# Optimization experiments

Measured on AMD Instinct MI355X. Metric: run time of the kernel, lower is better.

Reference implementation:

```python
import jax, jax.numpy as jnp
import numpy as np

B, T, HID = 1, 2048, 1024
H, D, S, KMAX = 16, 64, 64, 8


def local_attention(q, k, v, W):
    # lucidrains LocalAttention: causal, look_backward=1, autopad, scale=D**-0.5
    b, h, t, d = q.shape
    pad = (-t) % W
    qp = jnp.pad(q, ((0, 0), (0, 0), (0, pad), (0, 0)))
    kp = jnp.pad(k, ((0, 0), (0, 0), (0, pad), (0, 0)))
    vp = jnp.pad(v, ((0, 0), (0, 0), (0, pad), (0, 0)))
    tp = t + pad
    nw = tp // W
    qw = qp.reshape(b, h, nw, W, d)
    kw = kp.reshape(b, h, nw, W, d)
    vw = vp.reshape(b, h, nw, W, d)

    def look_back(x):  # prepend previous window (zeros for window 0)
        prev = jnp.pad(x, ((0, 0), (0, 0), (1, 0), (0, 0), (0, 0)))[:, :, :nw]
        return jnp.concatenate([prev, x], axis=3)  # (b,h,nw,2W,d)

    kk, vv = look_back(kw), look_back(vw)
    pos = jnp.arange(tp).reshape(nw, W)
    kpos = jnp.concatenate(
        [jnp.pad(pos, ((1, 0), (0, 0)), constant_values=-1)[:nw], pos], axis=1)  # (nw,2W)
    scores = jnp.einsum('bhnwd,bhnkd->bhnwk', qw, kk) * (d ** -0.5)
    valid = (pos[:, :, None] >= kpos[:, None, :]) & (kpos[:, None, :] >= 0)
    scores = jnp.where(valid[None, None], scores, -jnp.finfo(scores.dtype).max)
    probs = jax.nn.softmax(scores, axis=-1)
    out = jnp.einsum('bhnwk,bhnkd->bhnwd', probs, vv).reshape(b, h, tp, d)
    return out[:, :, :t]


def setup_inputs() -> dict:
    key = jax.random.key(0)
    ks = jax.random.split(key, 9)
    sd = 0.02
    return {
        'hidden_states': jax.random.normal(ks[0], (B, T, HID), jnp.float32),
        'Wq': jax.random.normal(ks[1], (HID, H * D), jnp.float32) * sd,
        'Wk': jax.random.normal(ks[2], (HID, H * D), jnp.float32) * sd,
        'Wv': jax.random.normal(ks[3], (HID, H * D), jnp.float32) * sd,
        'Wo': jax.random.normal(ks[4], (H * D, HID), jnp.float32) * sd,
        'Wc': jax.random.normal(ks[5], (S * D, D), jnp.float32) * sd,
        'bc': jax.random.normal(ks[6], (D,), jnp.float32) * sd,
        'k_scale': jnp.ones((1, H, 1), jnp.float32),
        'k_bias': jnp.zeros((1, H, 1), jnp.float32),
        'Wg': jax.random.normal(ks[7], (HID, 3 * H), jnp.float32) * sd,
        'bg': jax.random.normal(ks[8], (3 * H,), jnp.float32) * sd,
    }


def reference(hidden_states, Wq, Wk, Wv, Wo, Wc, bc, k_scale, k_bias, Wg, bg):
    b, t, _ = hidden_states.shape
    scale = D ** -0.5
    q = (hidden_states @ Wq).reshape(b, t, H, D).transpose(0, 2, 1, 3)
    k = (hidden_states @ Wk).reshape(b, t, H, D).transpose(0, 2, 1, 3)
    v = (hidden_states @ Wv).reshape(b, t, H, D).transpose(0, 2, 1, 3)

    sw_out = local_attention(q, k, v, S)

    pad = (-t) % S
    qp = jnp.pad(q, ((0, 0), (0, 0), (0, pad), (0, 0)))
    kp = jnp.pad(k, ((0, 0), (0, 0), (0, pad), (0, 0)))
    vp = jnp.pad(v, ((0, 0), (0, 0), (0, pad), (0, 0)))
    tp = t + pad
    nb = tp // S

    # compressed branch: shared compress MLP for k and v (same weights in torch)
    k_blk = kp.reshape(b, H, nb, S * D)
    v_blk = vp.reshape(b, H, nb, S * D)
    kc = jax.nn.gelu(k_blk @ Wc + bc, approximate=False)  # (b,H,nb,D)
    vc = jax.nn.gelu(v_blk @ Wc + bc, approximate=False)

    importance = jnp.einsum('bhid,bhjd->bhij', qp, kc) * scale  # (b,H,tp,nb)
    comp_probs = jax.nn.softmax(importance, axis=-1)
    comp_out = jnp.einsum('bhij,bhjd->bhid', comp_probs, vc)[:, :, :t]

    # block scores, entropy-driven dynamic top-k
    block_scores = importance.reshape(b, H, nb, S, nb).mean(axis=3)  # (b,H,nb,nb)
    block_probs = jax.nn.softmax(block_scores, axis=-1)
    entropy = -jnp.sum(block_probs * jnp.log(block_probs + 1e-9), axis=-1)
    max_entropy = jnp.log(jnp.float32(nb))
    norm_entropy = entropy / (max_entropy + 1e-9)  # (b,H,nb)
    k_logit = k_scale * norm_entropy + k_bias
    k_ratio = jax.nn.sigmoid(k_logit)
    dynamic_k = jnp.clip(KMAX * k_ratio, 1, KMAX).astype(jnp.int32)
    avg_k = dynamic_k.astype(jnp.float32).mean()

    _, topk_idx = jax.lax.top_k(block_scores, KMAX)  # (b,H,nb,KMAX)
    k_mask = jnp.arange(KMAX)[None, None, None, :] < dynamic_k[..., None]
    sel = (topk_idx[..., None] == jnp.arange(nb)) & k_mask[..., None]  # (b,H,nb,K,nb)
    mask = sel.any(axis=-2) | jnp.eye(nb, dtype=bool)  # (b,H,nb,nb)
    sparse_mask = jnp.repeat(jnp.repeat(mask, S, axis=2), S, axis=3)  # (b,H,tp,tp)

    attn = jnp.einsum('bhid,bhjd->bhij', qp, kp) * scale
    attn = jnp.where(sparse_mask, attn, -jnp.finfo(attn.dtype).max)
    fine_probs = jax.nn.softmax(attn, axis=-1)
    fine_out = jnp.einsum('bhij,bhjd->bhid', fine_probs, vp)[:, :, :t]

    gate = jax.nn.sigmoid(hidden_states @ Wg + bg)  # (b,t,3H)
    gate = gate.reshape(b, t, H, 3).transpose(0, 2, 1, 3)  # (b,H,t,3)
    combined = jnp.stack([sw_out, comp_out, fine_out], axis=-1)  # (b,H,t,D,3)
    out = jnp.einsum('bhnds,bhns->bhnd', combined, gate)
    merged = out.transpose(0, 2, 1, 3).reshape(b, t, H * D)
    output = merged @ Wo
    return output, avg_k, k_ratio, norm_entropy
```

## Files before the change

kernel.cpp:

```cpp
#include <hip/hip_runtime.h>
#include <math.h>

#define TT 2048
#define NH 16
#define HD 64
#define NB 32
#define HIDDEN 1024

typedef short s8v __attribute__((ext_vector_type(8)));
typedef float f4v __attribute__((ext_vector_type(4)));

__device__ __forceinline__ unsigned short f2bf(float x){
  unsigned u = __float_as_uint(x);
  unsigned r = (u + 0x7fffu + ((u>>16)&1u)) >> 16;
  return (unsigned short)r;
}
__device__ __forceinline__ float bf2f(unsigned short b){
  return __uint_as_float(((unsigned)b)<<16);
}
__device__ __forceinline__ void bsplit(float x, unsigned short& h, unsigned short& l){
  h = f2bf(x);
  l = f2bf(x - bf2f(h));
}

__device__ __forceinline__ float rmax32(float v){
#pragma unroll
  for(int o=16;o>0;o>>=1) v = fmaxf(v, __shfl_xor(v,o,32));
  return v;
}
__device__ __forceinline__ float rsum32(float v){
#pragma unroll
  for(int o=16;o>0;o>>=1) v += __shfl_xor(v,o,32);
  return v;
}

__global__ __launch_bounds__(256) void prep_all(
    const float* __restrict__ hs,
    const float* __restrict__ Wq, const float* __restrict__ Wk,
    const float* __restrict__ Wv, const float* __restrict__ Wo,
    const float* __restrict__ Wc,
    const float* __restrict__ Wg, const float* __restrict__ bg,
    unsigned short* __restrict__ hh, unsigned short* __restrict__ hl,
    unsigned short* __restrict__ wth, unsigned short* __restrict__ wtl,
    unsigned short* __restrict__ woth,
    unsigned short* __restrict__ wcth, unsigned short* __restrict__ wctl,
    float* __restrict__ gatep)
{
  __shared__ float SL[64*68];
  int bx = blockIdx.x;
  int t = threadIdx.x;
  if(bx < 2048){
    int i = (bx*256 + t)*4;
    float4 x = *(const float4*)(hs + i);
    ushort4 hv, lv;
    bsplit(x.x, hv.x, lv.x); bsplit(x.y, hv.y, lv.y);
    bsplit(x.z, hv.z, lv.z); bsplit(x.w, hv.w, lv.w);
    *(ushort4*)(hh + i) = hv;
    *(ushort4*)(hl + i) = lv;
    return;
  }
  if(bx < 3072){
    float (*L)[68] = (float(*)[68])SL;
    int idx = bx - 2048;
    int z = idx>>8, ky = (idx>>4)&15, nx = idx&15;
    const float* W = (z==0)?Wq:((z==1)?Wk:((z==2)?Wv:Wo));
    int k0 = ky*64, n0 = nx*64;
    int rr = t>>2, cg = t&3;
    const float* src = W + (size_t)(k0+rr)*1024 + n0 + cg*16;
    float4 a = *(const float4*)(src);
    float4 b = *(const float4*)(src+4);
    float4 c = *(const float4*)(src+8);
    float4 d = *(const float4*)(src+12);
    *(float4*)&L[rr][cg*16+0]  = a;
    *(float4*)&L[rr][cg*16+4]  = b;
    *(float4*)&L[rr][cg*16+8]  = c;
    *(float4*)&L[rr][cg*16+12] = d;
    __syncthreads();
    int nr = t>>2, kg = t&3;
    unsigned short hb[16], lb[16];
#pragma unroll
    for(int j=0;j<16;j++){
      float v = L[kg*16+j][nr];
      bsplit(v, hb[j], lb[j]);
    }
    if(z<3){
      size_t orow = ((size_t)z*1024 + n0 + nr)*1024 + k0 + kg*16;
      *(ushort4*)(wth+orow+0)  = make_ushort4(hb[0],hb[1],hb[2],hb[3]);
      *(ushort4*)(wth+orow+4)  = make_ushort4(hb[4],hb[5],hb[6],hb[7]);
      *(ushort4*)(wth+orow+8)  = make_ushort4(hb[8],hb[9],hb[10],hb[11]);
      *(ushort4*)(wth+orow+12) = make_ushort4(hb[12],hb[13],hb[14],hb[15]);
      *(ushort4*)(wtl+orow+0)  = make_ushort4(lb[0],lb[1],lb[2],lb[3]);
      *(ushort4*)(wtl+orow+4)  = make_ushort4(lb[4],lb[5],lb[6],lb[7]);
      *(ushort4*)(wtl+orow+8)  = make_ushort4(lb[8],lb[9],lb[10],lb[11]);
      *(ushort4*)(wtl+orow+12) = make_ushort4(lb[12],lb[13],lb[14],lb[15]);
    }else{
      size_t orow = ((size_t)n0 + nr)*1024 + k0 + kg*16;
      *(ushort4*)(woth+orow+0)  = make_ushort4(hb[0],hb[1],hb[2],hb[3]);
      *(ushort4*)(woth+orow+4)  = make_ushort4(hb[4],hb[5],hb[6],hb[7]);
      *(ushort4*)(woth+orow+8)  = make_ushort4(hb[8],hb[9],hb[10],hb[11]);
      *(ushort4*)(woth+orow+12) = make_ushort4(hb[12],hb[13],hb[14],hb[15]);
    }
    return;
  }
  if(bx < 3136){
    float (*L)[68] = (float(*)[68])SL;
    int k0 = (bx - 3072)*64;
    int rr = t>>2, cg = t&3;
    const float* src = Wc + (size_t)(k0+rr)*64 + cg*16;
    float4 a = *(const float4*)(src);
    float4 b = *(const float4*)(src+4);
    float4 c = *(const float4*)(src+8);
    float4 d = *(const float4*)(src+12);
    *(float4*)&L[rr][cg*16+0]  = a;
    *(float4*)&L[rr][cg*16+4]  = b;
    *(float4*)&L[rr][cg*16+8]  = c;
    *(float4*)&L[rr][cg*16+12] = d;
    __syncthreads();
    int nr = t>>2, kg = t&3;
    unsigned short hb[16], lb[16];
#pragma unroll
    for(int j=0;j<16;j++){
      float v = L[kg*16+j][nr];
      bsplit(v, hb[j], lb[j]);
    }
    size_t orow = (size_t)nr*4096 + k0 + kg*16;
    *(ushort4*)(wcth+orow+0)  = make_ushort4(hb[0],hb[1],hb[2],hb[3]);
    *(ushort4*)(wcth+orow+4)  = make_ushort4(hb[4],hb[5],hb[6],hb[7]);
    *(ushort4*)(wcth+orow+8)  = make_ushort4(hb[8],hb[9],hb[10],hb[11]);
    *(ushort4*)(wcth+orow+12) = make_ushort4(hb[12],hb[13],hb[14],hb[15]);
    *(ushort4*)(wctl+orow+0)  = make_ushort4(lb[0],lb[1],lb[2],lb[3]);
    *(ushort4*)(wctl+orow+4)  = make_ushort4(lb[4],lb[5],lb[6],lb[7]);
    *(ushort4*)(wctl+orow+8)  = make_ushort4(lb[8],lb[9],lb[10],lb[11]);
    *(ushort4*)(wctl+orow+12) = make_ushort4(lb[12],lb[13],lb[14],lb[15]);
    return;
  }
  {
    float* row = SL;
    float (*red)[64] = (float(*)[64])(SL + 1024);
    int tr = bx - 3136;
    *(float4*)(row + t*4) = *(const float4*)(hs + (size_t)tr*HIDDEN + t*4);
    __syncthreads();
    int n = t & 63, part = t>>6;
    float s = 0.f;
    if(n < 48){
      const float* w = Wg + n;
      for(int kx = part*256; kx < part*256+256; kx++)
        s += row[kx]*w[(size_t)kx*48];
    }
    red[part][n] = s;
    __syncthreads();
    if(part==0 && n<48){
      float x = red[0][n]+red[1][n]+red[2][n]+red[3][n] + bg[n];
      gatep[(size_t)tr*48 + n] = 1.f/(1.f+expf(-x));
    }
  }
}

#define LROW 40
__global__ __launch_bounds__(256) void mfma_qkv_k(
    const unsigned short* __restrict__ ahg, const unsigned short* __restrict__ alg,
    const unsigned short* __restrict__ bhg, const unsigned short* __restrict__ blg,
    unsigned short* __restrict__ qbh, unsigned short* __restrict__ qbl,
    unsigned short* __restrict__ kbh, unsigned short* __restrict__ kbl,
    unsigned short* __restrict__ vbh)
{
  __shared__ unsigned short SH[15360];
  unsigned short* SA  = SH;
  unsigned short* SAl = SH + 5120;
  unsigned short* SB  = SH + 10240;
  unsigned short* SBl = SH + 12800;
  int tid = threadIdx.x;
  int bn = blockIdx.x*64, bm = blockIdx.y*128;
  bool tp = (blockIdx.x < 32);
  int aRow = tid>>1, aOff = (tid&1)*16;
  int bRow = tid>>2, bOff = (tid&3)*8;
  const unsigned short* gA  = ahg + (size_t)(bm+aRow)*HIDDEN + aOff;
  const unsigned short* gAl = alg + (size_t)(bm+aRow)*HIDDEN + aOff;
  const unsigned short* gB  = bhg + (size_t)(bn+bRow)*HIDDEN + bOff;
  const unsigned short* gBl = blg + (size_t)(bn+bRow)*HIDDEN + bOff;
  int wlA = aRow*LROW + aOff;
  int wlB = bRow*LROW + bOff;
  int wv = tid>>6, ln = tid&63;
  int wm = (wv&1)*64, wn = (wv>>1)*32;
  int fr = ln&15, fq = ln>>4;
  f4v acc[4][2] = {};
  for(int k0=0;k0<HIDDEN;k0+=32){
    s8v a0 = *(const s8v*)(gA + k0);
    s8v a1 = *(const s8v*)(gA + k0 + 8);
    s8v b0 = *(const s8v*)(gB + k0);
    s8v a0l, a1l, b0l;
    if(tp){
      a0l = *(const s8v*)(gAl + k0);
      a1l = *(const s8v*)(gAl + k0 + 8);
      b0l = *(const s8v*)(gBl + k0);
    }
    __syncthreads();
    *(s8v*)&SA[wlA] = a0; *(s8v*)&SA[wlA+8] = a1;
    *(s8v*)&SB[wlB] = b0;
    if(tp){
      *(s8v*)&SAl[wlA] = a0l; *(s8v*)&SAl[wlA+8] = a1l;
      *(s8v*)&SBl[wlB] = b0l;
    }
    __syncthreads();
    s8v af[4], bf[2], tf;
#pragma unroll
    for(int i=0;i<4;i++) af[i] = *(const s8v*)&SA[(wm+i*16+fr)*LROW + fq*8];
#pragma unroll
    for(int j=0;j<2;j++) bf[j] = *(const s8v*)&SB[(wn+j*16+fr)*LROW + fq*8];
#pragma unroll
    for(int i=0;i<4;i++)
#pragma unroll
      for(int j=0;j<2;j++)
        acc[i][j] = __builtin_amdgcn_mfma_f32_16x16x32_bf16(af[i], bf[j], acc[i][j], 0,0,0);
    if(tp){
#pragma unroll
      for(int i=0;i<4;i++){
        tf = *(const s8v*)&SAl[(wm+i*16+fr)*LROW + fq*8];
#pragma unroll
        for(int j=0;j<2;j++)
          acc[i][j] = __builtin_amdgcn_mfma_f32_16x16x32_bf16(tf, bf[j], acc[i][j], 0,0,0);
      }
#pragma unroll
      for(int j=0;j<2;j++){
        tf = *(const s8v*)&SBl[(wn+j*16+fr)*LROW + fq*8];
#pragma unroll
        for(int i=0;i<4;i++)
          acc[i][j] = __builtin_amdgcn_mfma_f32_16x16x32_bf16(af[i], tf, acc[i][j], 0,0,0);
      }
    }
  }
  int z = bn >> 10;
  int head = (bn & 1023) >> 6;
  unsigned short* Cs = SH;
  unsigned short* dsth = (z==0)?qbh:((z==1)?kbh:vbh);
  size_t obase = ((size_t)head*TT + bm)*HD;
  __syncthreads();
#pragma unroll
  for(int i=0;i<4;i++)
#pragma unroll
    for(int j=0;j<2;j++)
#pragma unroll
      for(int r=0;r<4;r++)
        Cs[(wm+i*16+fq*4+r)*64 + wn+j*16+fr] = f2bf(acc[i][j][r]);
  __syncthreads();
#pragma unroll
  for(int u=0;u<4;u++){
    int c = u*256 + tid;
    *(s8v*)(dsth + obase + c*8) = *(const s8v*)&Cs[c*8];
  }
  if(z<2){
    unsigned short* dstl = (z==0)?qbl:kbl;
    __syncthreads();
#pragma unroll
    for(int i=0;i<4;i++)
#pragma unroll
      for(int j=0;j<2;j++)
#pragma unroll
        for(int r=0;r<4;r++){
          float v = acc[i][j][r];
          Cs[(wm+i*16+fq*4+r)*64 + wn+j*16+fr] = f2bf(v - bf2f(f2bf(v)));
        }
    __syncthreads();
#pragma unroll
    for(int u=0;u<4;u++){
      int c = u*256 + tid;
      *(s8v*)(dstl + obase + c*8) = *(const s8v*)&Cs[c*8];
    }
  }
}

__global__ __launch_bounds__(256) void conv_vt(
    const unsigned short* __restrict__ vbh, unsigned short* __restrict__ vth)
{
  int tt = blockIdx.x, h = blockIdx.y;
  __shared__ unsigned short L[64][72];
  int t = threadIdx.x;
  int row = t>>2, dg = (t&3)*16;
  const unsigned short* src = vbh + ((size_t)h*TT + tt*64 + row)*HD + dg;
  *(s8v*)&L[row][dg]   = *(const s8v*)(src);
  *(s8v*)&L[row][dg+8] = *(const s8v*)(src+8);
  __syncthreads();
  int d = t>>2, kg = (t&3)*16;
  s8v r0, r1;
#pragma unroll
  for(int u=0;u<8;u++)  r0[u] = (short)L[kg+u][d];
#pragma unroll
  for(int u=0;u<8;u++)  r1[u] = (short)L[kg+8+u][d];
  unsigned short* dst = vth + ((size_t)h*HD + d)*TT + tt*64 + kg;
  *(s8v*)(dst)   = r0;
  *(s8v*)(dst+8) = r1;
}

#define CROW 40
__global__ __launch_bounds__(256) void mfma_compress_k(
    const unsigned short* __restrict__ kbh, const unsigned short* __restrict__ kbl,
    const unsigned short* __restrict__ vbh,
    const unsigned short* __restrict__ wcth, const unsigned short* __restrict__ wctl,
    float* __restrict__ ccpart)
{
  __shared__ unsigned short As[64*CROW], Al[64*CROW], Bs[64*CROW], Bl[64*CROW];
  int chunk = blockIdx.x;
  int mt = blockIdx.y;
  bool isK = (mt < 8);
  const unsigned short* Ag  = isK ? (kbh + (size_t)mt*262144) : (vbh + (size_t)(mt-8)*262144);
  const unsigned short* Agl = kbl + (size_t)(isK ? mt : 0)*262144;
  int tid = threadIdx.x;
  int sr = tid>>2, skg = (tid&3)*8;
  int k0b = chunk*512;
  const unsigned short* gA  = Ag  + (size_t)sr*4096 + k0b + skg;
  const unsigned short* gAl = Agl + (size_t)sr*4096 + k0b + skg;
  const unsigned short* gB  = wcth + (size_t)sr*4096 + k0b + skg;
  const unsigned short* gBl = wctl + (size_t)sr*4096 + k0b + skg;
  int wv = tid>>6, ln = tid&63;
  int fr = ln&15, fq = ln>>4;
  int wlds = sr*CROW + skg;
  f4v acc[4] = {};
  for(int ks=0; ks<512; ks+=32){
    s8v a0 = *(const s8v*)(gA + ks);
    s8v b0 = *(const s8v*)(gB + ks);
    s8v b1 = *(const s8v*)(gBl + ks);
    s8v a1 = {};
    if(isK) a1 = *(const s8v*)(gAl + ks);
    __syncthreads();
    *(s8v*)&As[wlds] = a0;
    *(s8v*)&Bs[wlds] = b0;
    *(s8v*)&Bl[wlds] = b1;
    if(isK) *(s8v*)&Al[wlds] = a1;
    __syncthreads();
    s8v bfh = *(const s8v*)&Bs[(wv*16+fr)*CROW + fq*8];
    s8v bfl = *(const s8v*)&Bl[(wv*16+fr)*CROW + fq*8];
#pragma unroll
    for(int m=0;m<4;m++){
      s8v af = *(const s8v*)&As[(m*16+fr)*CROW + fq*8];
      acc[m] = __builtin_amdgcn_mfma_f32_16x16x32_bf16(af, bfh, acc[m], 0,0,0);
      acc[m] = __builtin_amdgcn_mfma_f32_16x16x32_bf16(af, bfl, acc[m], 0,0,0);
      if(isK){
        s8v afl = *(const s8v*)&Al[(m*16+fr)*CROW + fq*8];
        acc[m] = __builtin_amdgcn_mfma_f32_16x16x32_bf16(afl, bfh, acc[m], 0,0,0);
      }
    }
  }
  float* dst = ccpart + ((size_t)chunk*1024 + mt*64)*64;
#pragma unroll
  for(int m=0;m<4;m++)
#pragma unroll
    for(int r=0;r<4;r++)
      dst[(size_t)(m*16+fq*4+r)*64 + wv*16 + fr] = acc[m][r];
}

__global__ __launch_bounds__(256) void compress_fin(
    const float* __restrict__ ccpart, const float* __restrict__ bcp,
    unsigned short* __restrict__ kch, unsigned short* __restrict__ kcl,
    unsigned short* __restrict__ vcth)
{
  int idx = blockIdx.x*256 + threadIdx.x;
  int row = idx>>6, col = idx&63;
  float s = 0.f;
#pragma unroll
  for(int c=0;c<8;c++) s += ccpart[(size_t)c*65536 + idx];
  s += bcp[col];
  float g = 0.5f*s*(1.f+erff(s*0.70710678118654752f));
  if(row < 512){
    unsigned short hi = f2bf(g);
    kch[idx] = hi;
    kcl[idx] = f2bf(g - bf2f(hi));
  }else{
    int r = row - 512;
    int h = r>>5, j = r&31;
    vcth[((size_t)h*64 + col)*32 + j] = f2bf(g);
  }
}

__global__ __launch_bounds__(256) void comp_attn_mfma(
    const unsigned short* __restrict__ qbh, const unsigned short* __restrict__ qbl,
    const unsigned short* __restrict__ kch, const unsigned short* __restrict__ kcl,
    const unsigned short* __restrict__ vcth,
    float* __restrict__ imp, float* __restrict__ comp)
{
  __shared__ unsigned short Pl[4*16*40];
  int tid = threadIdx.x;
  int wave = __builtin_amdgcn_readfirstlane(tid>>6);
  int ln = tid&63;
  int fr = ln&15, fq = ln>>4;
  int i = blockIdx.x, h = blockIdx.y;

  const unsigned short* qrh = qbh + ((size_t)h*TT + i*64 + wave*16 + fr)*HD + fq*8;
  const unsigned short* qrl = qbl + ((size_t)h*TT + i*64 + wave*16 + fr)*HD + fq*8;
  s8v bh0 = *(const s8v*)(qrh);
  s8v bh1 = *(const s8v*)(qrh + 32);
  s8v bl0 = *(const s8v*)(qrl);
  s8v bl1 = *(const s8v*)(qrl + 32);

  f4v sv[2] = {};
#pragma unroll
  for(int mt=0;mt<2;mt++){
    const unsigned short* ar = kch + ((size_t)h*32 + mt*16 + fr)*HD + fq*8;
    const unsigned short* al = kcl + ((size_t)h*32 + mt*16 + fr)*HD + fq*8;
    s8v ah0 = *(const s8v*)(ar);
    s8v ah1 = *(const s8v*)(ar + 32);
    s8v al0 = *(const s8v*)(al);
    s8v al1 = *(const s8v*)(al + 32);
    sv[mt] = __builtin_amdgcn_mfma_f32_16x16x32_bf16(ah0, bh0, sv[mt], 0,0,0);
    sv[mt] = __builtin_amdgcn_mfma_f32_16x16x32_bf16(ah1, bh1, sv[mt], 0,0,0);
    sv[mt] = __builtin_amdgcn_mfma_f32_16x16x32_bf16(al0, bh0, sv[mt], 0,0,0);
    sv[mt] = __builtin_amdgcn_mfma_f32_16x16x32_bf16(al1, bh1, sv[mt], 0,0,0);
    sv[mt] = __builtin_amdgcn_mfma_f32_16x16x32_bf16(ah0, bl0, sv[mt], 0,0,0);
    sv[mt] = __builtin_amdgcn_mfma_f32_16x16x32_bf16(ah1, bl1, sv[mt], 0,0,0);
  }
  int t = i*64 + wave*16 + fr;
  float* impr = imp + ((size_t)h*TT + t)*NB;
  float mx = -3.4e38f;
#pragma unroll
  for(int mt=0;mt<2;mt++)
#pragma unroll
    for(int r=0;r<4;r++){
      float s = sv[mt][r]*0.125f;
      sv[mt][r] = s;
      impr[mt*16 + fq*4 + r] = s;
      mx = fmaxf(mx, s);
    }
  mx = fmaxf(mx, __shfl_xor(mx,16,64));
  mx = fmaxf(mx, __shfl_xor(mx,32,64));
  unsigned short* Pw = Pl + wave*16*40;
  float es = 0.f;
#pragma unroll
  for(int mt=0;mt<2;mt++)
#pragma unroll
    for(int r=0;r<4;r++){
      float p = __expf(sv[mt][r] - mx);
      es += p;
      Pw[fr*40 + mt*16 + fq*4 + r] = f2bf(p);
    }
  es += __shfl_xor(es,16,64);
  es += __shfl_xor(es,32,64);

  s8v ap = *(const s8v*)&Pw[fr*40 + fq*8];
  f4v acc[4] = {};
#pragma unroll
  for(int nt=0;nt<4;nt++){
    s8v bv = *(const s8v*)(vcth + ((size_t)h*64 + nt*16 + fr)*32 + fq*8);
    acc[nt] = __builtin_amdgcn_mfma_f32_16x16x32_bf16(ap, bv, acc[nt], 0,0,0);
  }
  float lv[4];
#pragma unroll
  for(int r=0;r<4;r++) lv[r] = __shfl(es, fq*4+r, 64);
#pragma unroll
  for(int nt=0;nt<4;nt++)
#pragma unroll
    for(int r=0;r<4;r++){
      int tq = i*64 + wave*16 + fq*4 + r;
      comp[((size_t)h*TT + tq)*HD + nt*16 + fr] = acc[nt][r]/lv[r];
    }
}

__global__ __launch_bounds__(256) void block_stats(
    const float* __restrict__ imp, const float* __restrict__ ksc, const float* __restrict__ kbi,
    unsigned* __restrict__ maskb, float* __restrict__ dkf,
    float* __restrict__ out_kratio, float* __restrict__ out_nent)
{
  int hb = blockIdx.x; int h = hb>>5, i = hb&31;
  int tid = threadIdx.x; int j = tid&31, p = tid>>5;
  const float* base = imp + ((size_t)h*TT + i*64)*NB;
  float s = 0.f;
  for(int t2=p*8; t2<p*8+8; t2++) s += base[(size_t)t2*NB + j];
  __shared__ float red[8][32];
  red[p][j] = s;
  __syncthreads();
  if(tid < 32){
    float bs = 0.f;
#pragma unroll
    for(int pp=0; pp<8; pp++) bs += red[pp][j];
    bs *= (1.f/64.f);
    float m = rmax32(bs);
    float e = expf(bs - m);
    float se = rsum32(e);
    float prob = e/se;
    float ent = rsum32(-prob * logf(prob + 1e-9f));
    float nent = ent / (3.4657359027997265f + 1e-9f);
    float kl = ksc[h]*nent + kbi[h];
    float kr = 1.f/(1.f + expf(-kl));
    float dkfl = fminf(fmaxf(8.f*kr, 1.f), 8.f);
    int dk = (int)dkfl;
    unsigned sel = 0u;
    for(int r=0;r<dk;r++){
      bool unpicked = ((sel>>j)&1u)==0u;
      float cand = unpicked ? bs : -3.4e38f;
      float mx = rmax32(cand);
      unsigned long long b = __ballot(cand == mx);
      int idxsel = __ffsll(b & 0xffffffffull) - 1;
      sel |= (1u<<idxsel);
    }
    sel |= (1u<<i);
    if(j==0){
      maskb[hb] = sel;
      dkf[hb] = (float)dk;
      out_kratio[hb] = kr;
      out_nent[hb] = nent;
    }
  }
}

__global__ __launch_bounds__(256) void avgk_kernel(const float* __restrict__ dkf, float* __restrict__ outp){
  __shared__ float red[256];
  int tid=threadIdx.x;
  red[tid] = dkf[tid] + dkf[tid+256];
  __syncthreads();
  for(int s=128;s>0;s>>=1){ if(tid<s) red[tid]+=red[tid+s]; __syncthreads(); }
  if(tid==0) outp[0] = red[0] * (1.f/512.f);
}

__global__ __launch_bounds__(256) void attn_fused(
    const unsigned short* __restrict__ qbh, const unsigned short* __restrict__ kbh,
    const unsigned short* __restrict__ vth, const unsigned* __restrict__ maskb,
    const float* __restrict__ comp, const float* __restrict__ gatep,
    unsigned short* __restrict__ mergedh)
{
  __shared__ unsigned short Kb[64*72];
  __shared__ unsigned short Vt[64*72];
  __shared__ unsigned short Pf[4*16*72];
  __shared__ unsigned short Ps[4*16*72];
  int tid = threadIdx.x;
  int wave = __builtin_amdgcn_readfirstlane(tid>>6);
  int ln = tid & 63;
  int fr = ln & 15, fq = ln >> 4;
  int hb = blockIdx.x; int h = hb>>5, i = hb&31;
  unsigned mb_s = (1u<<i) | (i ? (1u<<(i-1)) : 0u);
  unsigned mb_f = maskb[hb];
  unsigned mb = mb_s | mb_f;

  const unsigned short* qrow = qbh + ((size_t)h*TT + i*64 + wave*16 + fr)*HD + fq*8;
  s8v bq0 = *(const s8v*)(qrow);
  s8v bq1 = *(const s8v*)(qrow + 32);

  f4v acc_f[4] = {}, acc_s[4] = {};
  float mf = -3.4e38f, lf = 0.f, ms = -3.4e38f, ls = 0.f;

  int srow = tid>>2, sg = (tid&3)*16;
  unsigned short* Pfw = Pf + wave*16*72;
  unsigned short* Psw = Ps + wave*16*72;
  int qpos = wave*16 + fr;

  for(int j=0;j<NB;j++){
    if(!((mb>>j)&1u)) continue;
    __syncthreads();
    {
      const unsigned short* ks_ = kbh + ((size_t)h*TT + j*64 + srow)*HD + sg;
      *(s8v*)&Kb[srow*72 + sg]     = *(const s8v*)(ks_);
      *(s8v*)&Kb[srow*72 + sg + 8] = *(const s8v*)(ks_ + 8);
      const unsigned short* vs_ = vth + ((size_t)h*HD + srow)*TT + j*64 + sg;
      *(s8v*)&Vt[srow*72 + sg]     = *(const s8v*)(vs_);
      *(s8v*)&Vt[srow*72 + sg + 8] = *(const s8v*)(vs_ + 8);
    }
    __syncthreads();

    f4v sv[4] = {};
#pragma unroll
    for(int mt=0;mt<4;mt++){
      s8v ak0 = *(const s8v*)&Kb[(mt*16+fr)*72 + fq*8];
      s8v ak1 = *(const s8v*)&Kb[(mt*16+fr)*72 + fq*8 + 32];
      sv[mt] = __builtin_amdgcn_mfma_f32_16x16x32_bf16(ak0, bq0, sv[mt], 0,0,0);
      sv[mt] = __builtin_amdgcn_mfma_f32_16x16x32_bf16(ak1, bq1, sv[mt], 0,0,0);
    }
#pragma unroll
    for(int mt=0;mt<4;mt++)
#pragma unroll
      for(int r=0;r<4;r++) sv[mt][r] *= 0.125f;

    bool in_f = ((mb_f>>j)&1u) != 0u;
    bool in_s = (j==i) || (j+1==i);

    if(in_f){
      float mx = -3.4e38f;
#pragma unroll
      for(int mt=0;mt<4;mt++)
#pragma unroll
        for(int r=0;r<4;r++) mx = fmaxf(mx, sv[mt][r]);
      mx = fmaxf(mx, __shfl_xor(mx,16,64));
      mx = fmaxf(mx, __shfl_xor(mx,32,64));
      float mnew = fmaxf(mf, mx);
      float es = 0.f;
#pragma unroll
      for(int mt=0;mt<4;mt++)
#pragma unroll
        for(int r=0;r<4;r++){
          float p = __expf(sv[mt][r] - mnew);
          es += p;
          Pfw[fr*72 + mt*16 + fq*4 + r] = f2bf(p);
        }
      es += __shfl_xor(es,16,64);
      es += __shfl_xor(es,32,64);
      float alpha = __expf(mf - mnew);
      lf = lf*alpha + es;
      mf = mnew;
      float av[4];
#pragma unroll
      for(int r=0;r<4;r++) av[r] = __shfl(alpha, fq*4+r, 64);
#pragma unroll
      for(int nt=0;nt<4;nt++)
#pragma unroll
        for(int r=0;r<4;r++) acc_f[nt][r] *= av[r];
    }
    if(in_s){
      if(j==i){
#pragma unroll
        for(int mt=0;mt<4;mt++)
#pragma unroll
          for(int r=0;r<4;r++)
            if((mt*16 + fq*4 + r) > qpos) sv[mt][r] = -3.4e38f;
      }
      float mx = -3.4e38f;
#pragma unroll
      for(int mt=0;mt<4;mt++)
#pragma unroll
        for(int r=0;r<4;r++) mx = fmaxf(mx, sv[mt][r]);
      mx = fmaxf(mx, __shfl_xor(mx,16,64));
      mx = fmaxf(mx, __shfl_xor(mx,32,64));
      float mnew = fmaxf(ms, mx);
      float es = 0.f;
#pragma unroll
      for(int mt=0;mt<4;mt++)
#pragma unroll
        for(int r=0;r<4;r++){
          float p = __expf(sv[mt][r] - mnew);
          es += p;
          Psw[fr*72 + mt*16 + fq*4 + r] = f2bf(p);
        }
      es += __shfl_xor(es,16,64);
      es += __shfl_xor(es,32,64);
      float alpha = __expf(ms - mnew);
      ls = ls*alpha + es;
      ms = mnew;
      float av[4];
#pragma unroll
      for(int r=0;r<4;r++) av[r] = __shfl(alpha, fq*4+r, 64);
#pragma unroll
      for(int nt=0;nt<4;nt++)
#pragma unroll
        for(int r=0;r<4;r++) acc_s[nt][r] *= av[r];
    }

    if(in_f){
      s8v ap0 = *(const s8v*)&Pfw[fr*72 + fq*8];
      s8v ap1 = *(const s8v*)&Pfw[fr*72 + fq*8 + 32];
#pragma unroll
      for(int nt=0;nt<4;nt++){
        s8v bv0 = *(const s8v*)&Vt[(nt*16+fr)*72 + fq*8];
        s8v bv1 = *(const s8v*)&Vt[(nt*16+fr)*72 + fq*8 + 32];
        acc_f[nt] = __builtin_amdgcn_mfma_f32_16x16x32_bf16(ap0, bv0, acc_f[nt], 0,0,0);
        acc_f[nt] = __builtin_amdgcn_mfma_f32_16x16x32_bf16(ap1, bv1, acc_f[nt], 0,0,0);
      }
    }
    if(in_s){
      s8v ap0 = *(const s8v*)&Psw[fr*72 + fq*8];
      s8v ap1 = *(const s8v*)&Psw[fr*72 + fq*8 + 32];
#pragma unroll
      for(int nt=0;nt<4;nt++){
        s8v bv0 = *(const s8v*)&Vt[(nt*16+fr)*72 + fq*8];
        s8v bv1 = *(const s8v*)&Vt[(nt*16+fr)*72 + fq*8 + 32];
        acc_s[nt] = __builtin_amdgcn_mfma_f32_16x16x32_bf16(ap0, bv0, acc_s[nt], 0,0,0);
        acc_s[nt] = __builtin_amdgcn_mfma_f32_16x16x32_bf16(ap1, bv1, acc_s[nt], 0,0,0);
      }
    }
  }

  float lvf[4], lvs[4], g0[4], g1[4], g2[4];
#pragma unroll
  for(int r=0;r<4;r++){
    lvf[r] = __shfl(lf, fq*4+r, 64);
    lvs[r] = __shfl(ls, fq*4+r, 64);
    int t = i*64 + wave*16 + fq*4 + r;
    const float* g = gatep + (size_t)t*48 + h*3;
    g0[r] = g[0]; g1[r] = g[1]; g2[r] = g[2];
  }
#pragma unroll
  for(int nt=0;nt<4;nt++){
#pragma unroll
    for(int r=0;r<4;r++){
      int t = i*64 + wave*16 + fq*4 + r;
      int d = nt*16 + fr;
      float of = acc_f[nt][r] / lvf[r];
      float os = acc_s[nt][r] / lvs[r];
      float cp = comp[((size_t)h*TT + t)*HD + d];
      mergedh[(size_t)t*1024 + h*64 + d] = f2bf(g0[r]*os + g1[r]*cp + g2[r]*of);
    }
  }
}

__global__ __launch_bounds__(256) void mfma_proj_k(
    const unsigned short* __restrict__ ahg, const unsigned short* __restrict__ bhg,
    float* __restrict__ C)
{
  __shared__ unsigned short SA[128*LROW], SB[64*LROW];
  int tid = threadIdx.x;
  int bn = blockIdx.x*64, bm = blockIdx.y*128;
  int aRow = tid>>1, aOff = (tid&1)*16;
  int bRow = tid>>2, bOff = (tid&3)*8;
  const unsigned short* gA = ahg + (size_t)(bm+aRow)*HIDDEN + aOff;
  const unsigned short* gB = bhg + (size_t)(bn+bRow)*HIDDEN + bOff;
  int wlA = aRow*LROW + aOff;
  int wlB = bRow*LROW + bOff;
  int wv = tid>>6, ln = tid&63;
  int wm = (wv&1)*64, wn = (wv>>1)*32;
  int fr = ln&15, fq = ln>>4;
  f4v acc[4][2] = {};
  for(int k0=0;k0<HIDDEN;k0+=32){
    s8v a0 = *(const s8v*)(gA + k0);
    s8v a1 = *(const s8v*)(gA + k0 + 8);
    s8v b0 = *(const s8v*)(gB + k0);
    __syncthreads();
    *(s8v*)&SA[wlA] = a0; *(s8v*)&SA[wlA+8] = a1;
    *(s8v*)&SB[wlB] = b0;
    __syncthreads();
    s8v af[4], bf[2];
#pragma unroll
    for(int i=0;i<4;i++) af[i] = *(const s8v*)&SA[(wm+i*16+fr)*LROW + fq*8];
#pragma unroll
    for(int j=0;j<2;j++) bf[j] = *(const s8v*)&SB[(wn+j*16+fr)*LROW + fq*8];
#pragma unroll
    for(int i=0;i<4;i++)
#pragma unroll
      for(int j=0;j<2;j++)
        acc[i][j] = __builtin_amdgcn_mfma_f32_16x16x32_bf16(af[i], bf[j], acc[i][j], 0,0,0);
  }
#pragma unroll
  for(int i=0;i<4;i++){
    int mb = bm + wm + i*16 + fq*4;
#pragma unroll
    for(int j=0;j<2;j++){
      int n = bn + wn + j*16 + fr;
      float* dst = C + (size_t)mb*HIDDEN + n;
#pragma unroll
      for(int r=0;r<4;r++) dst[(size_t)r*HIDDEN] = acc[i][j][r];
    }
  }
}

extern "C" void kernel_launch(void* const* d_in, const int* in_sizes, int n_in,
                              void* d_out, int out_size, void* d_ws, size_t ws_size,
                              hipStream_t stream) {
  (void)in_sizes; (void)n_in; (void)out_size; (void)ws_size;
  const float* hs  = (const float*)d_in[0];
  const float* Wq  = (const float*)d_in[1];
  const float* Wk  = (const float*)d_in[2];
  const float* Wv  = (const float*)d_in[3];
  const float* Wo  = (const float*)d_in[4];
  const float* Wc  = (const float*)d_in[5];
  const float* bcp = (const float*)d_in[6];
  const float* ksc = (const float*)d_in[7];
  const float* kbi = (const float*)d_in[8];
  const float* Wg  = (const float*)d_in[9];
  const float* bg  = (const float*)d_in[10];
  float* out = (float*)d_out;

  float* ws = (float*)d_ws;
  float* gatep  = ws;
  unsigned short* kch  = (unsigned short*)(gatep + 98304);
  unsigned short* kcl  = kch + 32768;
  unsigned short* vcth = kcl + 32768;
  float* imp    = gatep + 98304 + 65536;
  float* comp   = imp + 1048576;
  float* wthf   = comp + 2097152;
  float* wtlf   = wthf + 1572864;
  unsigned short* mergedh = (unsigned short*)(wtlf + 1572864);
  float* dkf    = wtlf + 1572864 + 1048576;
  unsigned* maskb = (unsigned*)(dkf + 512);
  unsigned short* woth = (unsigned short*)(dkf + 1024);
  unsigned short* qbh  = (unsigned short*)(dkf + 1024 + 524288);
  unsigned short* qbl  = qbh + 2097152;
  unsigned short* kbh  = qbl + 2097152;
  unsigned short* kbl  = kbh + 2097152;
  unsigned short* vbh  = kbl + 2097152;
  unsigned short* vth  = vbh + 2097152;
  unsigned short* wcth = vth + 2097152;
  unsigned short* wctl = wcth + 262144;
  float* ccpart = (float*)(wctl + 262144);

  unsigned short* hsh = (unsigned short*)comp;
  unsigned short* hsl = (unsigned short*)(comp + 1048576);
  unsigned short* wth = (unsigned short*)wthf;
  unsigned short* wtl = (unsigned short*)wtlf;

  float* out_avgk   = out + 2097152;
  float* out_kratio = out + 2097153;
  float* out_nent   = out + 2097665;

  prep_all<<<dim3(5184), 256, 0, stream>>>(hs, Wq, Wk, Wv, Wo, Wc, Wg, bg,
                                           hsh, hsl, wth, wtl, woth, wcth, wctl, gatep);
  mfma_qkv_k<<<dim3(48,16), 256, 0, stream>>>(hsh, hsl, wth, wtl,
                                              qbh, qbl, kbh, kbl, vbh);
  conv_vt<<<dim3(32,16), 256, 0, stream>>>(vbh, vth);
  mfma_compress_k<<<dim3(8,16), 256, 0, stream>>>(kbh, kbl, vbh, wcth, wctl, ccpart);
  compress_fin<<<dim3(256), 256, 0, stream>>>(ccpart, bcp, kch, kcl, vcth);
  comp_attn_mfma<<<dim3(32,16), 256, 0, stream>>>(qbh, qbl, kch, kcl, vcth, imp, comp);
  block_stats<<<dim3(512), 256, 0, stream>>>(imp, ksc, kbi, maskb, dkf, out_kratio, out_nent);
  avgk_kernel<<<dim3(1), 256, 0, stream>>>(dkf, out_avgk);
  attn_fused<<<dim3(512), 256, 0, stream>>>(qbh, kbh, vth, maskb, comp, gatep, mergedh);
  mfma_proj_k<<<dim3(16,16), 256, 0, stream>>>(mergedh, woth, out);
}
```

Before: 223.7 us.

## Fuse V transpose, block stats and avg-k into producer kernels; pad LDS rows

Folds the V transpose into the QKV GEMM epilogue, so conv_vt and the vbh round trip are no longer needed for vth. Computes block importance column sums inside comp_attn_mfma, which removes the imp buffer and the block_stats kernel. Replaces the avgk reduction kernel with an atomicAdd, with the output zeroed in prep_all. Also changes the LDS row padding and the global-to-LDS load mapping in the GEMMs to cut bank conflicts. The atomic float sum makes avg_k depend on summation order.

```diff
diff --git a/kernel.cpp b/kernel.cpp
--- a/kernel.cpp
+++ b/kernel.cpp
@@ -44,11 +44,12 @@
     unsigned short* __restrict__ wth, unsigned short* __restrict__ wtl,
     unsigned short* __restrict__ woth,
     unsigned short* __restrict__ wcth, unsigned short* __restrict__ wctl,
-    float* __restrict__ gatep)
+    float* __restrict__ gatep, float* __restrict__ out_avgk)
 {
   __shared__ float SL[64*68];
   int bx = blockIdx.x;
   int t = threadIdx.x;
+  if(bx==0 && t==0) out_avgk[0] = 0.f;
   if(bx < 2048){
     int i = (bx*256 + t)*4;
     float4 x = *(const float4*)(hs + i);
@@ -156,50 +157,48 @@
   }
 }
 
-#define LROW 40
+#define LROW 48
 __global__ __launch_bounds__(256) void mfma_qkv_k(
     const unsigned short* __restrict__ ahg, const unsigned short* __restrict__ alg,
     const unsigned short* __restrict__ bhg, const unsigned short* __restrict__ blg,
     unsigned short* __restrict__ qbh, unsigned short* __restrict__ qbl,
     unsigned short* __restrict__ kbh, unsigned short* __restrict__ kbl,
-    unsigned short* __restrict__ vbh)
+    unsigned short* __restrict__ vbh, unsigned short* __restrict__ vth)
 {
-  __shared__ unsigned short SH[15360];
+  __shared__ unsigned short SH[18432];
   unsigned short* SA  = SH;
-  unsigned short* SAl = SH + 5120;
-  unsigned short* SB  = SH + 10240;
-  unsigned short* SBl = SH + 12800;
+  unsigned short* SAl = SH + 6144;
+  unsigned short* SB  = SH + 12288;
+  unsigned short* SBl = SH + 15360;
   int tid = threadIdx.x;
   int bn = blockIdx.x*64, bm = blockIdx.y*128;
   bool tp = (blockIdx.x < 32);
-  int aRow = tid>>1, aOff = (tid&1)*16;
-  int bRow = tid>>2, bOff = (tid&3)*8;
-  const unsigned short* gA  = ahg + (size_t)(bm+aRow)*HIDDEN + aOff;
-  const unsigned short* gAl = alg + (size_t)(bm+aRow)*HIDDEN + aOff;
-  const unsigned short* gB  = bhg + (size_t)(bn+bRow)*HIDDEN + bOff;
-  const unsigned short* gBl = blg + (size_t)(bn+bRow)*HIDDEN + bOff;
-  int wlA = aRow*LROW + aOff;
-  int wlB = bRow*LROW + bOff;
+  int sr = tid>>2, skg = (tid&3)*8;
+  const unsigned short* gA  = ahg + (size_t)(bm+sr)*HIDDEN + skg;
+  const unsigned short* gAl = alg + (size_t)(bm+sr)*HIDDEN + skg;
+  const unsigned short* gB  = bhg + (size_t)(bn+sr)*HIDDEN + skg;
+  const unsigned short* gBl = blg + (size_t)(bn+sr)*HIDDEN + skg;
+  int wlds = sr*LROW + skg;
   int wv = tid>>6, ln = tid&63;
   int wm = (wv&1)*64, wn = (wv>>1)*32;
   int fr = ln&15, fq = ln>>4;
   f4v acc[4][2] = {};
   for(int k0=0;k0<HIDDEN;k0+=32){
     s8v a0 = *(const s8v*)(gA + k0);
-    s8v a1 = *(const s8v*)(gA + k0 + 8);
+    s8v a1 = *(const s8v*)(gA + 65536 + k0);
     s8v b0 = *(const s8v*)(gB + k0);
     s8v a0l, a1l, b0l;
     if(tp){
       a0l = *(const s8v*)(gAl + k0);
-      a1l = *(const s8v*)(gAl + k0 + 8);
+      a1l = *(const s8v*)(gAl + 65536 + k0);
       b0l = *(const s8v*)(gBl + k0);
     }
     __syncthreads();
-    *(s8v*)&SA[wlA] = a0; *(s8v*)&SA[wlA+8] = a1;
-    *(s8v*)&SB[wlB] = b0;
+    *(s8v*)&SA[wlds] = a0; *(s8v*)&SA[wlds + 64*LROW] = a1;
+    *(s8v*)&SB[wlds] = b0;
     if(tp){
-      *(s8v*)&SAl[wlA] = a0l; *(s8v*)&SAl[wlA+8] = a1l;
-      *(s8v*)&SBl[wlB] = b0l;
+      *(s8v*)&SAl[wlds] = a0l; *(s8v*)&SAl[wlds + 64*LROW] = a1l;
+      *(s8v*)&SBl[wlds] = b0l;
     }
     __syncthreads();
     s8v af[4], bf[2], tf;
@@ -241,12 +240,12 @@
     for(int j=0;j<2;j++)
 #pragma unroll
       for(int r=0;r<4;r++)
-        Cs[(wm+i*16+fq*4+r)*64 + wn+j*16+fr] = f2bf(acc[i][j][r]);
+        Cs[(wm+i*16+fq*4+r)*72 + wn+j*16+fr] = f2bf(acc[i][j][r]);
   __syncthreads();
 #pragma unroll
   for(int u=0;u<4;u++){
     int c = u*256 + tid;
-    *(s8v*)(dsth + obase + c*8) = *(const s8v*)&Cs[c*8];
+    *(s8v*)(dsth + obase + c*8) = *(const s8v*)&Cs[(c>>3)*72 + (c&7)*8];
   }
   if(z<2){
     unsigned short* dstl = (z==0)?qbl:kbl;
@@ -258,40 +257,33 @@
 #pragma unroll
         for(int r=0;r<4;r++){
           float v = acc[i][j][r];
-          Cs[(wm+i*16+fq*4+r)*64 + wn+j*16+fr] = f2bf(v - bf2f(f2bf(v)));
+          Cs[(wm+i*16+fq*4+r)*72 + wn+j*16+fr] = f2bf(v - bf2f(f2bf(v)));
         }
     __syncthreads();
 #pragma unroll
     for(int u=0;u<4;u++){
       int c = u*256 + tid;
-      *(s8v*)(dstl + obase + c*8) = *(const s8v*)&Cs[c*8];
-    }
-  }
-}
-
-__global__ __launch_bounds__(256) void conv_vt(
-    const unsigned short* __restrict__ vbh, unsigned short* __restrict__ vth)
-{
-  int tt = blockIdx.x, h = blockIdx.y;
-  __shared__ unsigned short L[64][72];
-  int t = threadIdx.x;
-  int row = t>>2, dg = (t&3)*16;
-  const unsigned short* src = vbh + ((size_t)h*TT + tt*64 + row)*HD + dg;
-  *(s8v*)&L[row][dg]   = *(const s8v*)(src);
-  *(s8v*)&L[row][dg+8] = *(const s8v*)(src+8);
-  __syncthreads();
-  int d = t>>2, kg = (t&3)*16;
-  s8v r0, r1;
-#pragma unroll
-  for(int u=0;u<8;u++)  r0[u] = (short)L[kg+u][d];
-#pragma unroll
-  for(int u=0;u<8;u++)  r1[u] = (short)L[kg+8+u][d];
-  unsigned short* dst = vth + ((size_t)h*HD + d)*TT + tt*64 + kg;
-  *(s8v*)(dst)   = r0;
-  *(s8v*)(dst+8) = r1;
-}
-
-#define CROW 40
+      *(s8v*)(dstl + obase + c*8) = *(const s8v*)&Cs[(c>>3)*72 + (c&7)*8];
+    }
+  }else{
+    int d = tid>>2, tg = (tid&3)*32;
+    s8v r0,r1,r2,r3;
+#pragma unroll
+    for(int u=0;u<8;u++){
+      r0[u] = (short)Cs[(tg+u)*72 + d];
+      r1[u] = (short)Cs[(tg+8+u)*72 + d];
+      r2[u] = (short)Cs[(tg+16+u)*72 + d];
+      r3[u] = (short)Cs[(tg+24+u)*72 + d];
+    }
+    unsigned short* dv = vth + ((size_t)head*HD + d)*TT + bm + tg;
+    *(s8v*)(dv)    = r0;
+    *(s8v*)(dv+8)  = r1;
+    *(s8v*)(dv+16) = r2;
+    *(s8v*)(dv+24) = r3;
+  }
+}
+
+#define CROW 48
 __global__ __launch_bounds__(256) void mfma_compress_k(
     const unsigned short* __restrict__ kbh, const unsigned short* __restrict__ kbl,
     const unsigned short* __restrict__ vbh,
@@ -375,9 +367,12 @@
     const unsigned short* __restrict__ qbh, const unsigned short* __restrict__ qbl,
     const unsigned short* __restrict__ kch, const unsigned short* __restrict__ kcl,
     const unsigned short* __restrict__ vcth,
-    float* __restrict__ imp, float* __restrict__ comp)
+    const float* __restrict__ ksc, const float* __restrict__ kbi,
+    float* __restrict__ comp, unsigned* __restrict__ maskb,
+    float* __restrict__ out_avgk, float* __restrict__ out_kratio, float* __restrict__ out_nent)
 {
   __shared__ unsigned short Pl[4*16*40];
+  __shared__ float colsum[4][32];
   int tid = threadIdx.x;
   int wave = __builtin_amdgcn_readfirstlane(tid>>6);
   int ln = tid&63;
@@ -407,70 +402,30 @@
     sv[mt] = __builtin_amdgcn_mfma_f32_16x16x32_bf16(ah0, bl0, sv[mt], 0,0,0);
     sv[mt] = __builtin_amdgcn_mfma_f32_16x16x32_bf16(ah1, bl1, sv[mt], 0,0,0);
   }
-  int t = i*64 + wave*16 + fr;
-  float* impr = imp + ((size_t)h*TT + t)*NB;
-  float mx = -3.4e38f;
 #pragma unroll
   for(int mt=0;mt<2;mt++)
 #pragma unroll
-    for(int r=0;r<4;r++){
-      float s = sv[mt][r]*0.125f;
-      sv[mt][r] = s;
-      impr[mt*16 + fq*4 + r] = s;
-      mx = fmaxf(mx, s);
-    }
-  mx = fmaxf(mx, __shfl_xor(mx,16,64));
-  mx = fmaxf(mx, __shfl_xor(mx,32,64));
-  unsigned short* Pw = Pl + wave*16*40;
-  float es = 0.f;
+    for(int r=0;r<4;r++) sv[mt][r] *= 0.125f;
+
+  float cs[8];
 #pragma unroll
   for(int mt=0;mt<2;mt++)
 #pragma unroll
-    for(int r=0;r<4;r++){
-      float p = __expf(sv[mt][r] - mx);
-      es += p;
-      Pw[fr*40 + mt*16 + fq*4 + r] = f2bf(p);
-    }
-  es += __shfl_xor(es,16,64);
-  es += __shfl_xor(es,32,64);
-
-  s8v ap = *(const s8v*)&Pw[fr*40 + fq*8];
-  f4v acc[4] = {};
-#pragma unroll
-  for(int nt=0;nt<4;nt++){
-    s8v bv = *(const s8v*)(vcth + ((size_t)h*64 + nt*16 + fr)*32 + fq*8);
-    acc[nt] = __builtin_amdgcn_mfma_f32_16x16x32_bf16(ap, bv, acc[nt], 0,0,0);
-  }
-  float lv[4];
-#pragma unroll
-  for(int r=0;r<4;r++) lv[r] = __shfl(es, fq*4+r, 64);
-#pragma unroll
-  for(int nt=0;nt<4;nt++)
-#pragma unroll
-    for(int r=0;r<4;r++){
-      int tq = i*64 + wave*16 + fq*4 + r;
-      comp[((size_t)h*TT + tq)*HD + nt*16 + fr] = acc[nt][r]/lv[r];
-    }
-}
-
-__global__ __launch_bounds__(256) void block_stats(
-    const float* __restrict__ imp, const float* __restrict__ ksc, const float* __restrict__ kbi,
-    unsigned* __restrict__ maskb, float* __restrict__ dkf,
-    float* __restrict__ out_kratio, float* __restrict__ out_nent)
-{
-  int hb = blockIdx.x; int h = hb>>5, i = hb&31;
-  int tid = threadIdx.x; int j = tid&31, p = tid>>5;
-  const float* base = imp + ((size_t)h*TT + i*64)*NB;
-  float s = 0.f;
-  for(int t2=p*8; t2<p*8+8; t2++) s += base[(size_t)t2*NB + j];
-  __shared__ float red[8][32];
-  red[p][j] = s;
+    for(int r=0;r<4;r++) cs[mt*4+r] = sv[mt][r];
+#pragma unroll
+  for(int o=1;o<16;o<<=1)
+#pragma unroll
+    for(int u=0;u<8;u++) cs[u] += __shfl_xor(cs[u], o, 64);
+  if(fr==0){
+#pragma unroll
+    for(int mt=0;mt<2;mt++)
+#pragma unroll
+      for(int r=0;r<4;r++) colsum[wave][mt*16 + fq*4 + r] = cs[mt*4+r];
+  }
   __syncthreads();
-  if(tid < 32){
-    float bs = 0.f;
-#pragma unroll
-    for(int pp=0; pp<8; pp++) bs += red[pp][j];
-    bs *= (1.f/64.f);
+  if(wave==0 && ln<32){
+    int j = ln;
+    float bs = (colsum[0][j]+colsum[1][j]+colsum[2][j]+colsum[3][j]) * (1.f/64.f);
     float m = rmax32(bs);
     float e = expf(bs - m);
     float se = rsum32(e);
@@ -492,21 +447,51 @@
     }
     sel |= (1u<<i);
     if(j==0){
+      int hb = h*32 + i;
       maskb[hb] = sel;
-      dkf[hb] = (float)dk;
       out_kratio[hb] = kr;
       out_nent[hb] = nent;
-    }
-  }
-}
-
-__global__ __launch_bounds__(256) void avgk_kernel(const float* __restrict__ dkf, float* __restrict__ outp){
-  __shared__ float red[256];
-  int tid=threadIdx.x;
-  red[tid] = dkf[tid] + dkf[tid+256];
-  __syncthreads();
-  for(int s=128;s>0;s>>=1){ if(tid<s) red[tid]+=red[tid+s]; __syncthreads(); }
-  if(tid==0) outp[0] = red[0] * (1.f/512.f);
+      atomicAdd(out_avgk, (float)dk * (1.f/512.f));
+    }
+  }
+
+  float mx = -3.4e38f;
+#pragma unroll
+  for(int mt=0;mt<2;mt++)
+#pragma unroll
+    for(int r=0;r<4;r++) mx = fmaxf(mx, sv[mt][r]);
+  mx = fmaxf(mx, __shfl_xor(mx,16,64));
+  mx = fmaxf(mx, __shfl_xor(mx,32,64));
+  unsigned short* Pw = Pl + wave*16*40;
+  float es = 0.f;
+#pragma unroll
+  for(int mt=0;mt<2;mt++)
+#pragma unroll
+    for(int r=0;r<4;r++){
+      float p = __expf(sv[mt][r] - mx);
+      es += p;
+      Pw[fr*40 + mt*16 + fq*4 + r] = f2bf(p);
+    }
+  es += __shfl_xor(es,16,64);
+  es += __shfl_xor(es,32,64);
+
+  s8v ap = *(const s8v*)&Pw[fr*40 + fq*8];
+  f4v acc[4] = {};
+#pragma unroll
+  for(int nt=0;nt<4;nt++){
+    s8v bv = *(const s8v*)(vcth + ((size_t)h*64 + nt*16 + fr)*32 + fq*8);
+    acc[nt] = __builtin_amdgcn_mfma_f32_16x16x32_bf16(ap, bv, acc[nt], 0,0,0);
+  }
+  float lv[4];
+#pragma unroll
+  for(int r=0;r<4;r++) lv[r] = __shfl(es, fq*4+r, 64);
+#pragma unroll
+  for(int nt=0;nt<4;nt++)
+#pragma unroll
+    for(int r=0;r<4;r++){
+      int tq = i*64 + wave*16 + fq*4 + r;
+      comp[((size_t)h*TT + tq)*HD + nt*16 + fr] = acc[nt][r]/lv[r];
+    }
 }
 
 __global__ __launch_bounds__(256) void attn_fused(
@@ -693,23 +678,21 @@
   __shared__ unsigned short SA[128*LROW], SB[64*LROW];
   int tid = threadIdx.x;
   int bn = blockIdx.x*64, bm = blockIdx.y*128;
-  int aRow = tid>>1, aOff = (tid&1)*16;
-  int bRow = tid>>2, bOff = (tid&3)*8;
-  const unsigned short* gA = ahg + (size_t)(bm+aRow)*HIDDEN + aOff;
-  const unsigned short* gB = bhg + (size_t)(bn+bRow)*HIDDEN + bOff;
-  int wlA = aRow*LROW + aOff;
-  int wlB = bRow*LROW + bOff;
+  int sr = tid>>2, skg = (tid&3)*8;
+  const unsigned short* gA = ahg + (size_t)(bm+sr)*HIDDEN + skg;
+  const unsigned short* gB = bhg + (size_t)(bn+sr)*HIDDEN + skg;
+  int wlds = sr*LROW + skg;
   int wv = tid>>6, ln = tid&63;
   int wm = (wv&1)*64, wn = (wv>>1)*32;
   int fr = ln&15, fq = ln>>4;
   f4v acc[4][2] = {};
   for(int k0=0;k0<HIDDEN;k0+=32){
     s8v a0 = *(const s8v*)(gA + k0);
-    s8v a1 = *(const s8v*)(gA + k0 + 8);
+    s8v a1 = *(const s8v*)(gA + 65536 + k0);
     s8v b0 = *(const s8v*)(gB + k0);
     __syncthreads();
-    *(s8v*)&SA[wlA] = a0; *(s8v*)&SA[wlA+8] = a1;
-    *(s8v*)&SB[wlB] = b0;
+    *(s8v*)&SA[wlds] = a0; *(s8v*)&SA[wlds + 64*LROW] = a1;
+    *(s8v*)&SB[wlds] = b0;
     __syncthreads();
     s8v af[4], bf[2];
 #pragma unroll
@@ -757,15 +740,13 @@
   unsigned short* kch  = (unsigned short*)(gatep + 98304);
   unsigned short* kcl  = kch + 32768;
   unsigned short* vcth = kcl + 32768;
-  float* imp    = gatep + 98304 + 65536;
-  float* comp   = imp + 1048576;
+  float* comp   = gatep + 98304 + 65536;
   float* wthf   = comp + 2097152;
   float* wtlf   = wthf + 1572864;
   unsigned short* mergedh = (unsigned short*)(wtlf + 1572864);
-  float* dkf    = wtlf + 1572864 + 1048576;
-  unsigned* maskb = (unsigned*)(dkf + 512);
-  unsigned short* woth = (unsigned short*)(dkf + 1024);
-  unsigned short* qbh  = (unsigned short*)(dkf + 1024 + 524288);
+  unsigned* maskb = (unsigned*)(wtlf + 1572864 + 1048576);
+  unsigned short* woth = (unsigned short*)(wtlf + 1572864 + 1048576 + 512);
+  unsigned short* qbh  = woth + 1048576;
   unsigned short* qbl  = qbh + 2097152;
   unsigned short* kbh  = qbl + 2097152;
   unsigned short* kbl  = kbh + 2097152;
@@ -785,15 +766,15 @@
   float* out_nent   = out + 2097665;
 
   prep_all<<<dim3(5184), 256, 0, stream>>>(hs, Wq, Wk, Wv, Wo, Wc, Wg, bg,
-                                           hsh, hsl, wth, wtl, woth, wcth, wctl, gatep);
+                                           hsh, hsl, wth, wtl, woth, wcth, wctl,
+                                           gatep, out_avgk);
   mfma_qkv_k<<<dim3(48,16), 256, 0, stream>>>(hsh, hsl, wth, wtl,
-                                              qbh, qbl, kbh, kbl, vbh);
-  conv_vt<<<dim3(32,16), 256, 0, stream>>>(vbh, vth);
+                                              qbh, qbl, kbh, kbl, vbh, vth);
   mfma_compress_k<<<dim3(8,16), 256, 0, stream>>>(kbh, kbl, vbh, wcth, wctl, ccpart);
   compress_fin<<<dim3(256), 256, 0, stream>>>(ccpart, bcp, kch, kcl, vcth);
-  comp_attn_mfma<<<dim3(32,16), 256, 0, stream>>>(qbh, qbl, kch, kcl, vcth, imp, comp);
-  block_stats<<<dim3(512), 256, 0, stream>>>(imp, ksc, kbi, maskb, dkf, out_kratio, out_nent);
-  avgk_kernel<<<dim3(1), 256, 0, stream>>>(dkf, out_avgk);
+  comp_attn_mfma<<<dim3(32,16), 256, 0, stream>>>(qbh, qbl, kch, kcl, vcth,
+                                                  ksc, kbi, comp, maskb,
+                                                  out_avgk, out_kratio, out_nent);
   attn_fused<<<dim3(512), 256, 0, stream>>>(qbh, kbh, vth, maskb, comp, gatep, mergedh);
   mfma_proj_k<<<dim3(16,16), 256, 0, stream>>>(mergedh, woth, out);
 }
```

New measurement: 219.4 us. No clear change (-1.9%).
